# Optimization experiments

Measured on AMD Instinct MI355X. Metric: run time of the kernel, lower is better.

Reference implementation:

```python
import jax, jax.numpy as jnp
import numpy as np

NUM_HEADS = 16

def rotate_half(x):
    x1, x2 = jnp.split(x, 2, axis=-1)
    return jnp.concatenate((-x2, x1), axis=-1)

def setup_inputs() -> dict:
    key = jax.random.key(0)
    ks = jax.random.split(key, 5)
    b, n, dim, hd = 2, 2048, 1024, 64
    return {
        "x": jax.random.normal(ks[0], (b, n, dim), dtype=jnp.float32),
        "Wqkv": jax.random.normal(ks[1], (3 * dim, dim), dtype=jnp.float32) * (dim ** -0.5),
        "Wproj": jax.random.normal(ks[2], (dim, dim), dtype=jnp.float32) * (dim ** -0.5),
        "bproj": jnp.zeros((dim,), dtype=jnp.float32),
        "sin": jax.random.normal(ks[3], (n, hd), dtype=jnp.float32),
        "cos": jax.random.normal(ks[4], (n, hd), dtype=jnp.float32),
    }

def reference(x, Wqkv, Wproj, bproj, sin, cos):
    b, n, dim = x.shape
    h = NUM_HEADS
    d = dim // h
    qkv = x @ Wqkv.T
    qkv = qkv.reshape(b, n, 3, h, d).transpose(2, 0, 3, 1, 4)
    q, k, v = qkv[0], qkv[1], qkv[2]
    # RoPE: sin/cos [n, d] broadcast over [b, h, n, d]
    q = q * cos + rotate_half(q) * sin
    k = k * cos + rotate_half(k) * sin
    # SDPA (non-causal, no dropout at eval)
    scale = d ** -0.5
    scores = jnp.einsum("bhnd,bhmd->bhnm", q, k) * scale
    attn = jax.nn.softmax(scores, axis=-1)
    out = jnp.einsum("bhnm,bhmd->bhnd", attn, v)
    # merge heads: [b, h, n, d] -> [b, n, h*d]
    out = out.transpose(0, 2, 1, 3).reshape(b, n, dim)
    return out @ Wproj.T + bproj
```

## Files before the change

kernel.cpp:

```cpp
#include <hip/hip_runtime.h>
#include <hip/hip_fp16.h>

typedef _Float16 f16;
typedef _Float16 half8 __attribute__((ext_vector_type(8)));
typedef _Float16 half4v __attribute__((ext_vector_type(4)));
typedef float f32x4 __attribute__((ext_vector_type(4)));

#define QSCALE 0.18033688011112042f
#define SHIFT2 17.312340490667560f

__device__ __forceinline__ void gload_lds16(const void* g, void* lds) {
  __builtin_amdgcn_global_load_lds(
      (__attribute__((address_space(1))) void*)g,
      (__attribute__((address_space(3))) void*)lds, 16, 0, 0);
}

__global__ __launch_bounds__(256) void cvt_f32_f16_kernel(
    const float* __restrict__ src, f16* __restrict__ dst, int n4) {
  int i = blockIdx.x * 256 + threadIdx.x;
  if (i >= n4) return;
  float4 v = ((const float4*)src)[i];
  half4v o;
  o.x = (f16)v.x; o.y = (f16)v.y; o.z = (f16)v.z; o.w = (f16)v.w;
  ((half4v*)dst)[i] = o;
}

template<int EPI>
__global__ __launch_bounds__(256) void hgemm_kernel(
    const f16* __restrict__ A16, const f16* __restrict__ B, int K,
    const float* __restrict__ cosT, const float* __restrict__ sinT,
    f16* __restrict__ Qout, f16* __restrict__ Kout, f16* __restrict__ Vtout,
    const float* __restrict__ bias, float* __restrict__ Cout) {
  constexpr int BN = (EPI == 0) ? 128 : 64;
  constexpr int NJ = (EPI == 0) ? 4 : 2;
  __shared__ f16 As[2][128 * 32];
  __shared__ f16 Bs[2][BN * 32];
  const int tid = threadIdx.x;
  const int lane = tid & 63, w = tid >> 6;
  const int fr = lane & 15, fkg = lane >> 4;
  const int wm = (w >> 1) * 64;
  const int wn = (EPI == 0) ? (w & 1) * 64 : (w & 1) * 16;
  const long long rowBase = (long long)blockIdx.x * 128;
  const long long colBase = (long long)blockIdx.y * BN;

  f32x4 acc[4][NJ] = {};
  const f16* Ab = A16 + rowBase * K;
  const f16* Bb = B + colBase * K;

  const int srow = lane >> 2;
  const int kcol = ((lane & 3) ^ ((lane >> 3) & 3)) * 8;
  const int sw = (fkg ^ ((fr >> 1) & 3)) * 8;

  auto stage = [&](int buf, int k0) {
#pragma unroll
    for (int r = 0; r < 2; ++r) {
      int c = r * 4 + w;
      gload_lds16(Ab + (long long)(c * 16 + srow) * K + k0 + kcol, &As[buf][c * 512]);
    }
    if (EPI == 0) {
#pragma unroll
      for (int r = 0; r < 2; ++r) {
        int c = r * 4 + w;
        gload_lds16(Bb + (long long)(c * 16 + srow) * K + k0 + kcol, &Bs[buf][c * 512]);
      }
    } else {
      int c = w;
      gload_lds16(Bb + (long long)(c * 16 + srow) * K + k0 + kcol, &Bs[buf][c * 512]);
    }
  };

  stage(0, 0);
  for (int k0 = 0; k0 < K; k0 += 32) {
    const int buf = (k0 >> 5) & 1;
    __syncthreads();
    if (k0 + 32 < K) stage(buf ^ 1, k0 + 32);
    half8 a[4], b[NJ];
#pragma unroll
    for (int i = 0; i < 4; ++i)
      a[i] = *(const half8*)(&As[buf][((wm >> 4) + i) * 512 + fr * 32 + sw]);
#pragma unroll
    for (int j = 0; j < NJ; ++j) {
      int chunk = (EPI == 0) ? ((wn >> 4) + j) : ((wn >> 4) + j * 2);
      b[j] = *(const half8*)(&Bs[buf][chunk * 512 + fr * 32 + sw]);
    }
#pragma unroll
    for (int i = 0; i < 4; ++i)
#pragma unroll
      for (int j = 0; j < NJ; ++j)
        acc[i][j] = __builtin_amdgcn_mfma_f32_16x16x32_f16(a[i], b[j], acc[i][j], 0, 0, 0);
  }

  if (EPI == 0) {
#pragma unroll
    for (int i = 0; i < 4; ++i) {
#pragma unroll
      for (int r = 0; r < 4; ++r) {
        int rg = (int)rowBase + wm + i * 16 + fkg * 4 + r;
        int bidx = rg >> 11, nn = rg & 2047;
#pragma unroll
        for (int j = 0; j < 4; ++j) {
          int cg = (int)colBase + wn + j * 16 + fr;
          int t = cg >> 10, cc = cg & 1023;
          int head = cc >> 6, d = cc & 63;
          int bh = bidx * 16 + head;
          float v = acc[i][j][r];
          if (t == 2) {
            Vtout[((long long)bh * 64 + d) * 2048 + nn] = (f16)v;
          } else {
            float pal = acc[i][j ^ 2][r];
            float cs = cosT[nn * 64 + d];
            float sn = sinT[nn * 64 + d];
            v = v * cs + (d < 32 ? -pal : pal) * sn;
            if (t == 0) v *= QSCALE;
            f16 hv = (f16)v;
            if (t == 0) Qout[((long long)bh * 2048 + nn) * 64 + d] = hv;
            else        Kout[((long long)bh * 2048 + nn) * 64 + d] = hv;
          }
        }
      }
    }
  } else {
#pragma unroll
    for (int i = 0; i < 4; ++i)
#pragma unroll
      for (int r = 0; r < 4; ++r) {
        long long rg = rowBase + wm + i * 16 + fkg * 4 + r;
#pragma unroll
        for (int j = 0; j < NJ; ++j) {
          int cg = (int)colBase + wn + j * 32 + fr;
          Cout[rg * 1024 + cg] = acc[i][j][r] + bias[cg];
        }
      }
  }
}

__global__ __launch_bounds__(256) void attn_kernel(
    const f16* __restrict__ Q, const f16* __restrict__ Kb,
    const f16* __restrict__ Vt, f16* __restrict__ Om) {
  __shared__ f16 Ks[64 * 72];
  __shared__ f16 Vs[64 * 72];
  __shared__ f16 Ps[4][32 * 72];
  const int tid = threadIdx.x;
  const int lane = tid & 63, w = tid >> 6;
  const int fr = lane & 15, fkg = lane >> 4, fk = fkg * 8;
  const int bh = blockIdx.y;
  const int q0 = blockIdx.x * 128 + w * 32;
  f16* Psw = &Ps[w][0];

  half8 aq[2][2];
#pragma unroll
  for (int m = 0; m < 2; ++m)
#pragma unroll
    for (int ks = 0; ks < 2; ++ks)
      aq[m][ks] = *(const half8*)(Q + ((long long)bh * 2048 + q0 + m * 16 + fr) * 64 +
                                  ks * 32 + fk);

  half8 ones_frag;
#pragma unroll
  for (int j = 0; j < 8; ++j) ones_frag[j] = (fr == 0) ? (f16)1.0f : (f16)0.0f;

  f32x4 acc[2][5] = {};

  const int soff = tid * 8;
  const int skr0 = soff >> 6, sd0 = soff & 63;
  half8 kreg[2], vreg[2];
#pragma unroll
  for (int c = 0; c < 2; ++c) {
    int kr = skr0 + c * 32;
    kreg[c] = *(const half8*)(Kb + ((long long)bh * 2048 + kr) * 64 + sd0);
    vreg[c] = *(const half8*)(Vt + ((long long)bh * 64 + kr) * 2048 + sd0);
  }

  for (int kv0 = 0; kv0 < 2048; kv0 += 64) {
    __syncthreads();
#pragma unroll
    for (int c = 0; c < 2; ++c) {
      int kr = skr0 + c * 32;
      *(half8*)(Ks + kr * 72 + sd0) = kreg[c];
      *(half8*)(Vs + kr * 72 + sd0) = vreg[c];
    }
    if (kv0 + 64 < 2048) {
#pragma unroll
      for (int c = 0; c < 2; ++c) {
        int kr = skr0 + c * 32;
        kreg[c] = *(const half8*)(Kb + ((long long)bh * 2048 + kv0 + 64 + kr) * 64 + sd0);
        vreg[c] = *(const half8*)(Vt + ((long long)bh * 64 + kr) * 2048 + kv0 + 64 + sd0);
      }
    }
    __syncthreads();

    f32x4 z[2][4];
#pragma unroll
    for (int n = 0; n < 4; ++n) {
      half8 bk0 = *(const half8*)(Ks + (n * 16 + fr) * 72 + fk);
      half8 bk1 = *(const half8*)(Ks + (n * 16 + fr) * 72 + 32 + fk);
#pragma unroll
      for (int m = 0; m < 2; ++m) {
        f32x4 t = {0.f, 0.f, 0.f, 0.f};
        t = __builtin_amdgcn_mfma_f32_16x16x32_f16(bk0, aq[m][0], t, 0, 0, 0);
        t = __builtin_amdgcn_mfma_f32_16x16x32_f16(bk1, aq[m][1], t, 0, 0, 0);
        z[m][n] = t;
      }
    }

#pragma unroll
    for (int m = 0; m < 2; ++m)
#pragma unroll
      for (int n = 0; n < 4; ++n) {
        half4v h;
#pragma unroll
        for (int r = 0; r < 4; ++r)
          h[r] = (f16)__builtin_amdgcn_exp2f(z[m][n][r] - SHIFT2);
        *(half4v*)(Psw + (m * 16 + fr) * 72 + n * 16 + fkg * 4) = h;
      }

#pragma unroll
    for (int ks = 0; ks < 2; ++ks) {
      half8 ap[2];
#pragma unroll
      for (int m = 0; m < 2; ++m) {
        ap[m] = *(const half8*)(Psw + (m * 16 + fr) * 72 + ks * 32 + fk);
        acc[m][4] = __builtin_amdgcn_mfma_f32_16x16x32_f16(ap[m], ones_frag, acc[m][4], 0, 0, 0);
      }
#pragma unroll
      for (int dd = 0; dd < 4; ++dd) {
        half8 bv = *(const half8*)(Vs + (dd * 16 + fr) * 72 + ks * 32 + fk);
#pragma unroll
        for (int m = 0; m < 2; ++m)
          acc[m][dd] = __builtin_amdgcn_mfma_f32_16x16x32_f16(ap[m], bv, acc[m][dd], 0, 0, 0);
      }
    }
  }

  const int b = bh >> 4, h = bh & 15;
#pragma unroll
  for (int m = 0; m < 2; ++m)
#pragma unroll
    for (int r = 0; r < 4; ++r) {
      int nn = q0 + m * 16 + fkg * 4 + r;
      float l = __shfl(acc[m][4][r], lane & 48);
      float inv = 1.f / l;
#pragma unroll
      for (int dd = 0; dd < 4; ++dd)
        Om[((long long)b * 2048 + nn) * 1024 + h * 64 + dd * 16 + fr] =
            (f16)(acc[m][dd][r] * inv);
    }
}

extern "C" void kernel_launch(void* const* d_in, const int* in_sizes, int n_in,
                              void* d_out, int out_size, void* d_ws, size_t ws_size,
                              hipStream_t stream) {
  (void)in_sizes; (void)n_in; (void)out_size; (void)ws_size;
  const float* x     = (const float*)d_in[0];
  const float* Wqkv  = (const float*)d_in[1];
  const float* Wproj = (const float*)d_in[2];
  const float* bproj = (const float*)d_in[3];
  const float* sinT  = (const float*)d_in[4];
  const float* cosT  = (const float*)d_in[5];
  float* out = (float*)d_out;

  f16* ws     = (f16*)d_ws;
  f16* xh     = ws;
  f16* Om     = ws;
  f16* Wqkvh  = ws + 4194304;
  f16* Wprojh = ws + 7340032;
  f16* Qb     = ws + 8388608;
  f16* Kb     = ws + 12582912;
  f16* Vtb    = ws + 16777216;

  cvt_f32_f16_kernel<<<4096, 256, 0, stream>>>(x, xh, 1048576);
  cvt_f32_f16_kernel<<<3072, 256, 0, stream>>>(Wqkv, Wqkvh, 786432);
  cvt_f32_f16_kernel<<<1024, 256, 0, stream>>>(Wproj, Wprojh, 262144);

  hgemm_kernel<0><<<dim3(32, 24), 256, 0, stream>>>(
      xh, Wqkvh, 1024, cosT, sinT, Qb, Kb, Vtb, nullptr, nullptr);

  attn_kernel<<<dim3(16, 32), 256, 0, stream>>>(Qb, Kb, Vtb, Om);

  hgemm_kernel<1><<<dim3(32, 16), 256, 0, stream>>>(
      Om, Wprojh, 1024, nullptr, nullptr, nullptr, nullptr, nullptr, bproj, out);
}
```

Measured before the change: 133.0 us.

## Deepen GEMM prefetch to two stages and merge fp32-to-fp16 conversion launches

The three fp32-to-fp16 conversion launches become one kernel that picks the source buffer by thread index, which cuts launch overhead. The GEMM main loop now prefetches two K-tiles ahead. It uses explicit vmcnt waits and raw barriers, and reissues the next load into the current buffer only after its LDS reads have completed (lgkmcnt(0)), so global loads overlap the MFMA work. The hand-counted vmcnt values rely on the exact number of loads per stage, so the code is fragile if the staging changes.

```diff
diff --git a/kernel.cpp b/kernel.cpp
--- a/kernel.cpp
+++ b/kernel.cpp
@@ -15,14 +15,19 @@
       (__attribute__((address_space(3))) void*)lds, 16, 0, 0);
 }
 
-__global__ __launch_bounds__(256) void cvt_f32_f16_kernel(
-    const float* __restrict__ src, f16* __restrict__ dst, int n4) {
+__global__ __launch_bounds__(256) void cvt_all_kernel(
+    const float* __restrict__ x, const float* __restrict__ wqkv,
+    const float* __restrict__ wproj, f16* __restrict__ xh,
+    f16* __restrict__ wqkvh, f16* __restrict__ wprojh) {
   int i = blockIdx.x * 256 + threadIdx.x;
-  if (i >= n4) return;
-  float4 v = ((const float4*)src)[i];
+  const float* src; f16* dst; int off;
+  if (i < 1048576)      { src = x;     dst = xh;     off = i; }
+  else if (i < 1835008) { src = wqkv;  dst = wqkvh;  off = i - 1048576; }
+  else                  { src = wproj; dst = wprojh; off = i - 1835008; }
+  float4 v = ((const float4*)src)[off];
   half4v o;
   o.x = (f16)v.x; o.y = (f16)v.y; o.z = (f16)v.z; o.w = (f16)v.w;
-  ((half4v*)dst)[i] = o;
+  ((half4v*)dst)[off] = o;
 }
 
 template<int EPI>
@@ -69,11 +74,20 @@
     }
   };
 
+  const int NT = K >> 5;
   stage(0, 0);
-  for (int k0 = 0; k0 < K; k0 += 32) {
-    const int buf = (k0 >> 5) & 1;
-    __syncthreads();
-    if (k0 + 32 < K) stage(buf ^ 1, k0 + 32);
+  stage(1, 32);
+  for (int t = 0; t < NT; ++t) {
+    const int buf = t & 1;
+    const int k0 = t << 5;
+    if (t + 1 < NT) {
+      if constexpr (EPI == 0) asm volatile("s_waitcnt vmcnt(4)" ::: "memory");
+      else                    asm volatile("s_waitcnt vmcnt(3)" ::: "memory");
+    } else {
+      asm volatile("s_waitcnt vmcnt(0)" ::: "memory");
+    }
+    __builtin_amdgcn_s_barrier();
+    __builtin_amdgcn_sched_barrier(0);
     half8 a[4], b[NJ];
 #pragma unroll
     for (int i = 0; i < 4; ++i)
@@ -83,6 +97,10 @@
       int chunk = (EPI == 0) ? ((wn >> 4) + j) : ((wn >> 4) + j * 2);
       b[j] = *(const half8*)(&Bs[buf][chunk * 512 + fr * 32 + sw]);
     }
+    asm volatile("s_waitcnt lgkmcnt(0)" ::: "memory");
+    __builtin_amdgcn_sched_barrier(0);
+    __builtin_amdgcn_s_barrier();
+    if (t + 2 < NT) stage(buf, k0 + 64);
 #pragma unroll
     for (int i = 0; i < 4; ++i)
 #pragma unroll
@@ -268,9 +286,7 @@
   f16* Kb     = ws + 12582912;
   f16* Vtb    = ws + 16777216;
 
-  cvt_f32_f16_kernel<<<4096, 256, 0, stream>>>(x, xh, 1048576);
-  cvt_f32_f16_kernel<<<3072, 256, 0, stream>>>(Wqkv, Wqkvh, 786432);
-  cvt_f32_f16_kernel<<<1024, 256, 0, stream>>>(Wproj, Wprojh, 262144);
+  cvt_all_kernel<<<8192, 256, 0, stream>>>(x, Wqkv, Wproj, xh, Wqkvh, Wprojh);
 
   hgemm_kernel<0><<<dim3(32, 24), 256, 0, stream>>>(
       xh, Wqkvh, 1024, cosT, sinT, Qb, Kb, Vtb, nullptr, nullptr);
```

After: 126.1 us. 1.05x faster.
